# Performance work log

Measured on AMD Instinct MI355X. Metric: run time of the kernel, lower is better.

Reference implementation:

```python
import jax, jax.numpy as jnp
import numpy as np

B, A, M, C = 8, 120000, 32, 80
ALPHA, GAMMA = 0.25, 2.0


def setup_inputs() -> dict:
    key = jax.random.key(0)
    k1, k2, k3, k4, k5, k6, k7 = jax.random.split(key, 7)
    classifications = jax.random.uniform(k1, (B, A, C), jnp.float32, 1e-3, 1.0 - 1e-3)
    regressions = jax.random.normal(k2, (B, A, 4), jnp.float32)
    # anchors: valid boxes x1<x2, y1<y2 in a ~600px image
    axy1 = jax.random.uniform(k3, (1, A, 2), jnp.float32, 0.0, 550.0)
    awh = jax.random.uniform(k4, (1, A, 2), jnp.float32, 8.0, 64.0)
    anchors = jnp.concatenate([axy1, axy1 + awh], axis=-1)
    # annotations: [x1,y1,x2,y2,label], label in [0,C)
    gxy1 = jax.random.uniform(k5, (B, M, 2), jnp.float32, 0.0, 500.0)
    gwh = jax.random.uniform(k6, (B, M, 2), jnp.float32, 16.0, 100.0)
    labels = jax.random.randint(k7, (B, M, 1), 0, C).astype(jnp.float32)
    annotations = jnp.concatenate([gxy1, gxy1 + gwh, labels], axis=-1)
    return {"classifications": classifications, "regressions": regressions,
            "anchors": anchors, "annotations": annotations}


def _calc_iou(a, b):
    # a: [A,4] anchors, b: [M,4] gt boxes -> IoU [A,M]
    area = (b[:, 2] - b[:, 0]) * (b[:, 3] - b[:, 1])  # [M]
    iw = jnp.minimum(a[:, 2:3], b[None, :, 2]) - jnp.maximum(a[:, 0:1], b[None, :, 0])
    ih = jnp.minimum(a[:, 3:4], b[None, :, 3]) - jnp.maximum(a[:, 1:2], b[None, :, 1])
    inter = jnp.clip(iw, 0.0) * jnp.clip(ih, 0.0)
    ua = (a[:, 2] - a[:, 0])[:, None] * (a[:, 3] - a[:, 1])[:, None] + area[None, :] - inter
    return inter / jnp.clip(ua, 1e-8)


def reference(classifications, regressions, anchors, annotations):
    anchor = anchors[0]  # [A,4]
    aw = anchor[:, 2] - anchor[:, 0]
    ah = anchor[:, 3] - anchor[:, 1]
    acx = anchor[:, 0] + 0.5 * aw
    acy = anchor[:, 1] + 0.5 * ah

    def per_image(cls, reg, ann):
        cls = jnp.clip(cls, 1e-4, 1.0 - 1e-4)
        valid = ann[:, 4] != -1.0  # [M] padded gt filtered via mask
        iou = _calc_iou(anchor, ann[:, :4])  # [A,M]
        iou = jnp.where(valid[None, :], iou, -1.0)
        iou_max = iou.max(axis=1)  # [A]
        iou_argmax = iou.argmax(axis=1)
        pos = iou_max >= 0.5  # [A]
        num_pos = pos.sum()
        assigned = ann[iou_argmax]  # [A,5]
        labels = assigned[:, 4].astype(jnp.int32)

        # --- classification targets (-1 ignore, 0 background, 1 positive class) ---
        t = jnp.full_like(cls, -1.0)
        t = jnp.where((iou_max < 0.4)[:, None], 0.0, t)
        t = jnp.where(pos[:, None], 0.0, t)
        oh = jax.nn.one_hot(labels, C, dtype=jnp.bool_)
        t = jnp.where(pos[:, None] & oh, 1.0, t)

        # --- focal loss ---
        is_one = t == 1.0
        alpha_f = jnp.where(is_one, ALPHA, 1.0 - ALPHA)
        focal_w = alpha_f * jnp.where(is_one, 1.0 - cls, cls) ** GAMMA
        bce = -(t * jnp.log(cls) + (1.0 - t) * jnp.log(1.0 - cls))
        cls_loss = jnp.where(t != -1.0, focal_w * bce, 0.0)
        cls_l = cls_loss.sum() / jnp.maximum(num_pos.astype(jnp.float32), 1.0)

        gw = assigned[:, 2] - assigned[:, 0]
        gh = assigned[:, 3] - assigned[:, 1]
        gcx = assigned[:, 0] + 0.5 * gw
        gcy = assigned[:, 1] + 0.5 * gh
        gw = jnp.clip(gw, 1.0)
        gh = jnp.clip(gh, 1.0)
        tdx = (gcx - acx) / aw
        tdy = (gcy - acy) / ah
        tdw = jnp.log(gw / aw)
        tdh = jnp.log(gh / ah)
        targets = jnp.stack([tdx, tdy, tdw, tdh], axis=1) / jnp.array([[0.1, 0.1, 0.2, 0.2]], jnp.float32)
        diff = jnp.abs(targets - reg)  # [A,4]
        rloss = jnp.where(diff <= 1.0 / 9.0, 0.5 * 9.0 * diff * diff, diff - 0.5 / 9.0)
        rsum = jnp.sum(rloss * pos[:, None].astype(jnp.float32))
        npos_f = num_pos.astype(jnp.float32)
        reg_l = jnp.where(num_pos > 0, rsum / jnp.maximum(npos_f * 4.0, 1.0), 0.0)
        return cls_l, reg_l

    cls_ls, reg_ls = jax.vmap(per_image)(classifications, regressions, annotations)
    return jnp.mean(cls_ls, keepdims=True), jnp.mean(reg_ls, keepdims=True)
```

## Files before the change

kernel.cpp:

```cpp
#include <hip/hip_runtime.h>
#include <math.h>

#define NB 8
#define NA 120000
#define NM 32
#define NC 80

constexpr float ALPHA = 0.25f;
constexpr int TPB = 256;
constexpr int BLOCKS_PER_IMG = (NA + TPB - 1) / TPB;
constexpr float NEG_SCALE = 0.69314718056f * (1.0f - ALPHA);


__global__ __launch_bounds__(TPB, 4) void focal_main_kernel(
    const float* __restrict__ cls, const float* __restrict__ reg,
    const float* __restrict__ anc, const float* __restrict__ ann,
    float* __restrict__ ws) {
    const int blk = blockIdx.x;
    const int b = blk / BLOCKS_PER_IMG;
    const int ablk = blk % BLOCKS_PER_IMG;
    const int a0 = ablk * TPB;
    const int nA = min(TPB, NA - a0);
    const int t = threadIdx.x;

    __shared__ float s_ann[NM * 5];
    __shared__ int s_state[TPB];
    __shared__ float s_part[4][3];

    if (t < NM * 5) s_ann[t] = ann[b * NM * 5 + t];
    __syncthreads();

    float my_reg = 0.0f;
    float my_pos = 0.0f;

    if (t < nA) {
        const int a = a0 + t;
        const float4 ab = *(const float4*)(anc + a * 4);
        const float aw = ab.z - ab.x, ah = ab.w - ab.y;
        const float acx = ab.x + 0.5f * aw, acy = ab.y + 0.5f * ah;
        float best = -1e30f;
        int bi = 0;
#pragma unroll
        for (int m = 0; m < NM; ++m) {
            const float x1 = s_ann[m * 5 + 0], y1 = s_ann[m * 5 + 1];
            const float x2 = s_ann[m * 5 + 2], y2 = s_ann[m * 5 + 3];
            const float lb = s_ann[m * 5 + 4];
            const float area = (x2 - x1) * (y2 - y1);
            const float iw = fminf(ab.z, x2) - fmaxf(ab.x, x1);
            const float ih = fminf(ab.w, y2) - fmaxf(ab.y, y1);
            const float inter = fmaxf(iw, 0.0f) * fmaxf(ih, 0.0f);
            const float ua = aw * ah + area - inter;
            float iou = inter / fmaxf(ua, 1e-8f);
            if (lb == -1.0f) iou = -1.0f;
            if (iou > best) { best = iou; bi = m; }
        }
        const bool pos = (best >= 0.5f);
        int st;
        if (pos)              st = (int)s_ann[bi * 5 + 4];
        else if (best < 0.4f) st = -2;
        else                  st = -1;
        s_state[t] = st;

        if (pos) {
            my_pos = 1.0f;
            const float x1 = s_ann[bi * 5 + 0], y1 = s_ann[bi * 5 + 1];
            const float x2 = s_ann[bi * 5 + 2], y2 = s_ann[bi * 5 + 3];
            float gw = x2 - x1, gh = y2 - y1;
            const float gcx = x1 + 0.5f * gw, gcy = y1 + 0.5f * gh;
            gw = fmaxf(gw, 1.0f);
            gh = fmaxf(gh, 1.0f);
            const float tgt[4] = {
                (gcx - acx) / aw / 0.1f,
                (gcy - acy) / ah / 0.1f,
                __logf(gw / aw) / 0.2f,
                __logf(gh / ah) / 0.2f,
            };
            const float4 rg = *(const float4*)(reg + ((size_t)b * NA + a) * 4);
            const float rr[4] = { rg.x, rg.y, rg.z, rg.w };
#pragma unroll
            for (int k = 0; k < 4; ++k) {
                const float d = fabsf(tgt[k] - rr[k]);
                my_reg += (d <= 1.0f / 9.0f) ? 0.5f * 9.0f * d * d : d - 0.5f / 9.0f;
            }
        }
    } else {
        s_state[t] = -1;
    }
    __syncthreads();

    const float* cbase = cls + ((size_t)b * NA + a0) * NC;
    const int q0 = (t & 3) * 20;
    const int arow = t >> 2;
    const int npass = nA >> 6;

    float bg_acc = 0.0f;
    float pos_acc = 0.0f;

    for (int p = 0; p < npass; ++p) {
        const int idx = p * 64 + arow;
        const int st = s_state[idx];
        if (st == -1) continue;
        const float* ap = cbase + idx * NC + q0;
        const float4 r0 = *(const float4*)(ap + 0);
        const float4 r1 = *(const float4*)(ap + 4);
        const float4 r2 = *(const float4*)(ap + 8);
        const float4 r3 = *(const float4*)(ap + 12);
        const float4 r4 = *(const float4*)(ap + 16);
        if (st == -2) {
            const float4 rs[5] = { r0, r1, r2, r3, r4 };
#pragma unroll
            for (int i = 0; i < 5; ++i) {
                const float pv[4] = { rs[i].x, rs[i].y, rs[i].z, rs[i].w };
#pragma unroll
                for (int k = 0; k < 4; ++k) {
                    const float pp = pv[k];
                    bg_acc = fmaf(pp * pp, __log2f(1.0f - pp), bg_acc);
                }
            }
        } else {
            const float4 rs[5] = { r0, r1, r2, r3, r4 };
#pragma unroll
            for (int i = 0; i < 5; ++i) {
                const float pv[4] = { rs[i].x, rs[i].y, rs[i].z, rs[i].w };
#pragma unroll
                for (int k = 0; k < 4; ++k) {
                    const float pp = pv[k];
                    const bool one = (q0 + i * 4 + k) == st;
                    const float q = one ? 1.0f - pp : pp;
                    const float la = one ? pp : 1.0f - pp;
                    const float af = one ? ALPHA : 1.0f - ALPHA;
                    pos_acc += af * q * q * (-__logf(la));
                }
            }
        }
    }
    const float my_cls = pos_acc - NEG_SCALE * bg_acc;

    float v0 = my_cls, v1 = my_reg, v2 = my_pos;
#pragma unroll
    for (int off = 32; off > 0; off >>= 1) {
        v0 += __shfl_down(v0, off, 64);
        v1 += __shfl_down(v1, off, 64);
        v2 += __shfl_down(v2, off, 64);
    }
    const int wave = t >> 6;
    if ((t & 63) == 0) {
        s_part[wave][0] = v0; s_part[wave][1] = v1; s_part[wave][2] = v2;
    }
    __syncthreads();
    if (t == 0) {
        float c = 0.0f, r = 0.0f, pcnt = 0.0f;
#pragma unroll
        for (int w = 0; w < 4; ++w) { c += s_part[w][0]; r += s_part[w][1]; pcnt += s_part[w][2]; }
        float* slot = ws + (size_t)blk * 4;
        slot[0] = c; slot[1] = r; slot[2] = pcnt;
    }
}

__global__ __launch_bounds__(512) void finalize_kernel(const float* __restrict__ ws,
                                                       float* __restrict__ out) {
    const int t = threadIdx.x;
    const int w = t >> 6;
    const int l = t & 63;
    __shared__ float s_cls[NB], s_reg[NB];

    float c = 0.0f, r = 0.0f, p = 0.0f;
    for (int i = l; i < BLOCKS_PER_IMG; i += 64) {
        const float* slot = ws + ((size_t)w * BLOCKS_PER_IMG + i) * 4;
        c += slot[0]; r += slot[1]; p += slot[2];
    }
#pragma unroll
    for (int off = 32; off > 0; off >>= 1) {
        c += __shfl_down(c, off, 64);
        r += __shfl_down(r, off, 64);
        p += __shfl_down(p, off, 64);
    }
    if (l == 0) {
        s_cls[w] = c / fmaxf(p, 1.0f);
        s_reg[w] = (p > 0.0f) ? r / fmaxf(p * 4.0f, 1.0f) : 0.0f;
    }
    __syncthreads();
    if (t == 0) {
        float cs = 0.0f, rs = 0.0f;
#pragma unroll
        for (int b = 0; b < NB; ++b) { cs += s_cls[b]; rs += s_reg[b]; }
        out[0] = cs / (float)NB;
        out[1] = rs / (float)NB;
    }
}

extern "C" void kernel_launch(void* const* d_in, const int* in_sizes, int n_in,
                              void* d_out, int out_size, void* d_ws, size_t ws_size,
                              hipStream_t stream) {
    const float* cls = (const float*)d_in[0];
    const float* reg = (const float*)d_in[1];
    const float* anc = (const float*)d_in[2];
    const float* ann = (const float*)d_in[3];
    float* ws = (float*)d_ws;
    float* out = (float*)d_out;

    focal_main_kernel<<<NB * BLOCKS_PER_IMG, TPB, 0, stream>>>(cls, reg, anc, ann, ws);
    finalize_kernel<<<1, 512, 0, stream>>>(ws, out);
}
```

Before: 60.09 us.

## Software-pipeline classification loads with branchless focal loss and coalesced interleaved access

New measurement: 60.87 us. No clear change (+1.3%).

```diff
diff --git a/kernel.cpp b/kernel.cpp
--- a/kernel.cpp
+++ b/kernel.cpp
@@ -9,7 +9,7 @@
 constexpr float ALPHA = 0.25f;
 constexpr int TPB = 256;
 constexpr int BLOCKS_PER_IMG = (NA + TPB - 1) / TPB;
-constexpr float NEG_SCALE = 0.69314718056f * (1.0f - ALPHA);
+constexpr float LN2 = 0.69314718056f;
 
 
 __global__ __launch_bounds__(TPB, 4) void focal_main_kernel(
@@ -23,11 +23,16 @@
     const int nA = min(TPB, NA - a0);
     const int t = threadIdx.x;
 
-    __shared__ float s_ann[NM * 5];
+    __shared__ float4 s_box[NM];
+    __shared__ float s_lb[NM];
     __shared__ int s_state[TPB];
     __shared__ float s_part[4][3];
 
-    if (t < NM * 5) s_ann[t] = ann[b * NM * 5 + t];
+    if (t < NM) {
+        const float* ap = ann + (size_t)b * NM * 5 + (size_t)t * 5;
+        s_box[t] = make_float4(ap[0], ap[1], ap[2], ap[3]);
+        s_lb[t] = ap[4];
+    }
     __syncthreads();
 
     float my_reg = 0.0f;
@@ -38,35 +43,34 @@
         const float4 ab = *(const float4*)(anc + a * 4);
         const float aw = ab.z - ab.x, ah = ab.w - ab.y;
         const float acx = ab.x + 0.5f * aw, acy = ab.y + 0.5f * ah;
+        const float aarea = aw * ah;
         float best = -1e30f;
         int bi = 0;
 #pragma unroll
         for (int m = 0; m < NM; ++m) {
-            const float x1 = s_ann[m * 5 + 0], y1 = s_ann[m * 5 + 1];
-            const float x2 = s_ann[m * 5 + 2], y2 = s_ann[m * 5 + 3];
-            const float lb = s_ann[m * 5 + 4];
-            const float area = (x2 - x1) * (y2 - y1);
-            const float iw = fminf(ab.z, x2) - fmaxf(ab.x, x1);
-            const float ih = fminf(ab.w, y2) - fmaxf(ab.y, y1);
+            const float4 g = s_box[m];
+            const float lb = s_lb[m];
+            const float area = (g.z - g.x) * (g.w - g.y);
+            const float iw = fminf(ab.z, g.z) - fmaxf(ab.x, g.x);
+            const float ih = fminf(ab.w, g.w) - fmaxf(ab.y, g.y);
             const float inter = fmaxf(iw, 0.0f) * fmaxf(ih, 0.0f);
-            const float ua = aw * ah + area - inter;
+            const float ua = aarea + area - inter;
             float iou = inter / fmaxf(ua, 1e-8f);
             if (lb == -1.0f) iou = -1.0f;
             if (iou > best) { best = iou; bi = m; }
         }
         const bool pos = (best >= 0.5f);
         int st;
-        if (pos)              st = (int)s_ann[bi * 5 + 4];
+        if (pos)              st = (int)s_lb[bi];
         else if (best < 0.4f) st = -2;
         else                  st = -1;
         s_state[t] = st;
 
         if (pos) {
             my_pos = 1.0f;
-            const float x1 = s_ann[bi * 5 + 0], y1 = s_ann[bi * 5 + 1];
-            const float x2 = s_ann[bi * 5 + 2], y2 = s_ann[bi * 5 + 3];
-            float gw = x2 - x1, gh = y2 - y1;
-            const float gcx = x1 + 0.5f * gw, gcy = y1 + 0.5f * gh;
+            const float4 g = s_box[bi];
+            float gw = g.z - g.x, gh = g.w - g.y;
+            const float gcx = g.x + 0.5f * gw, gcy = g.y + 0.5f * gh;
             gw = fmaxf(gw, 1.0f);
             gh = fmaxf(gh, 1.0f);
             const float tgt[4] = {
@@ -89,52 +93,58 @@
     __syncthreads();
 
     const float* cbase = cls + ((size_t)b * NA + a0) * NC;
-    const int q0 = (t & 3) * 20;
     const int arow = t >> 2;
+    const int lq = t & 3;
     const int npass = nA >> 6;
-
-    float bg_acc = 0.0f;
-    float pos_acc = 0.0f;
-
-    for (int p = 0; p < npass; ++p) {
-        const int idx = p * 64 + arow;
-        const int st = s_state[idx];
-        if (st == -1) continue;
-        const float* ap = cbase + idx * NC + q0;
-        const float4 r0 = *(const float4*)(ap + 0);
-        const float4 r1 = *(const float4*)(ap + 4);
-        const float4 r2 = *(const float4*)(ap + 8);
-        const float4 r3 = *(const float4*)(ap + 12);
-        const float4 r4 = *(const float4*)(ap + 16);
-        if (st == -2) {
-            const float4 rs[5] = { r0, r1, r2, r3, r4 };
-#pragma unroll
-            for (int i = 0; i < 5; ++i) {
-                const float pv[4] = { rs[i].x, rs[i].y, rs[i].z, rs[i].w };
-#pragma unroll
-                for (int k = 0; k < 4; ++k) {
-                    const float pp = pv[k];
-                    bg_acc = fmaf(pp * pp, __log2f(1.0f - pp), bg_acc);
-                }
-            }
-        } else {
-            const float4 rs[5] = { r0, r1, r2, r3, r4 };
-#pragma unroll
-            for (int i = 0; i < 5; ++i) {
-                const float pv[4] = { rs[i].x, rs[i].y, rs[i].z, rs[i].w };
-#pragma unroll
-                for (int k = 0; k < 4; ++k) {
-                    const float pp = pv[k];
-                    const bool one = (q0 + i * 4 + k) == st;
-                    const float q = one ? 1.0f - pp : pp;
-                    const float la = one ? pp : 1.0f - pp;
-                    const float af = one ? ALPHA : 1.0f - ALPHA;
-                    pos_acc += af * q * q * (-__logf(la));
-                }
+    const float* base0 = cbase + (size_t)arow * NC + lq * 4;
+
+    const int st0 = s_state[arow];
+    const int st1 = s_state[64 + arow];
+    const int st2 = s_state[128 + arow];
+    const int st3 = (npass == 4) ? s_state[192 + arow] : -1;
+
+    float acc = 0.0f;
+
+#define LOADP(R, p) do { const float* _p = base0 + (size_t)(p) * 64 * NC;      \
+        R##0 = *(const float4*)(_p);      R##1 = *(const float4*)(_p + 16);    \
+        R##2 = *(const float4*)(_p + 32); R##3 = *(const float4*)(_p + 48);    \
+        R##4 = *(const float4*)(_p + 64); } while (0)
+
+    auto comp = [&](float4 r0, float4 r1, float4 r2, float4 r3, float4 r4, int st) {
+        const float maf_bg = (st == -1) ? 0.0f : (1.0f - ALPHA);
+        const float4 rs[5] = { r0, r1, r2, r3, r4 };
+#pragma unroll
+        for (int i = 0; i < 5; ++i) {
+            const float pv[4] = { rs[i].x, rs[i].y, rs[i].z, rs[i].w };
+#pragma unroll
+            for (int k = 0; k < 4; ++k) {
+                const float pp = pv[k];
+                const bool one = (lq * 4 + i * 16 + k) == st;
+                const float om = 1.0f - pp;
+                const float q  = one ? om : pp;
+                const float la = one ? pp : om;
+                const float maf = one ? ALPHA : maf_bg;
+                acc = fmaf(maf * q * q, __log2f(la), acc);
             }
         }
-    }
-    const float my_cls = pos_acc - NEG_SCALE * bg_acc;
+    };
+
+    float4 A0, A1, A2, A3, A4, B0, B1, B2, B3, B4;
+    if (npass == 4) {
+        LOADP(A, 0); LOADP(B, 1);
+        comp(A0, A1, A2, A3, A4, st0); LOADP(A, 2);
+        comp(B0, B1, B2, B3, B4, st1); LOADP(B, 3);
+        comp(A0, A1, A2, A3, A4, st2);
+        comp(B0, B1, B2, B3, B4, st3);
+    } else {
+        LOADP(A, 0); LOADP(B, 1);
+        comp(A0, A1, A2, A3, A4, st0); LOADP(A, 2);
+        comp(B0, B1, B2, B3, B4, st1);
+        comp(A0, A1, A2, A3, A4, st2);
+    }
+#undef LOADP
+
+    const float my_cls = -LN2 * acc;
 
     float v0 = my_cls, v1 = my_reg, v2 = my_pos;
 #pragma unroll
```
